# Kernel tuning notes

Measured on AMD Instinct MI355X. Metric: run time of the kernel, lower is better.

Reference implementation:

```python
import jax, jax.numpy as jnp
import numpy as np

N_EMBD = 1024
N_HEAD = 16
HEAD_DIM = N_EMBD // N_HEAD  # 64; scale = sqrt(64) = 8


def setup_inputs() -> dict:
    key = jax.random.key(0)
    k0, k1, k2, k3, k4 = jax.random.split(key, 5)
    B, T = 4, 2048
    x = jax.random.normal(k0, (B, T, N_EMBD), dtype=jnp.float32)
    # torch Linear weights are (out,in); we store (in,out) so y = x @ W + b
    W_attn = jax.random.normal(k1, (N_EMBD, 3 * N_EMBD), dtype=jnp.float32) * 0.02
    b_attn = jax.random.normal(k2, (3 * N_EMBD,), dtype=jnp.float32) * 0.02
    W_proj = jax.random.normal(k3, (N_EMBD, N_EMBD), dtype=jnp.float32) * 0.02
    b_proj = jax.random.normal(k4, (N_EMBD,), dtype=jnp.float32) * 0.02
    return {"x": x, "W_attn": W_attn, "b_attn": b_attn,
            "W_proj": W_proj, "b_proj": b_proj}


def reference(x, W_attn, b_attn, W_proj, b_proj):
    B, T, D = x.shape
    scale = 1.0 / np.float32(np.sqrt(HEAD_DIM))
    qkv = x @ W_attn + b_attn                      # [B,T,3D]
    q, k, v = jnp.split(qkv, 3, axis=-1)           # each [B,T,D]
    att = jnp.einsum('bid,bjd->bij', q, k) * scale # [B,T,T]
    causal = jnp.tril(jnp.ones((T, T), dtype=bool))
    att = jnp.where(causal[None, :, :], att, jnp.float32(-jnp.inf))
    att = jax.nn.softmax(att, axis=-1)
    y = jnp.einsum('bij,bjd->bid', att, v)         # [B,T,D]
    return y @ W_proj + b_proj
```

## Files before the change

kernel.cpp:

```cpp
#include <hip/hip_runtime.h>

typedef __attribute__((ext_vector_type(8))) short short8;
typedef __attribute__((ext_vector_type(4))) float f32x4;
typedef __attribute__((ext_vector_type(4))) unsigned short ushort4v;

struct DB0 { static constexpr int value = 0; };
struct DB1 { static constexpr int value = 1; };
struct DB2 { static constexpr int value = 2; };

__device__ __forceinline__ unsigned short f2bf(float f) {
  unsigned int u = __float_as_uint(f);
  u += 0x7fffu + ((u >> 16) & 1u);
  return (unsigned short)(u >> 16);
}
__device__ __forceinline__ float bf2f(unsigned short h) {
  return __uint_as_float(((unsigned int)h) << 16);
}

__device__ __forceinline__ void gload16(const unsigned short* g, unsigned short* l) {
  __builtin_amdgcn_global_load_lds(
      (const __attribute__((address_space(1))) unsigned int*)g,
      (__attribute__((address_space(3))) unsigned int*)l,
      16, 0, 0);
}

template <int OFF>
__device__ __forceinline__ short8 dsr(unsigned a) {
  short8 r;
  asm volatile("ds_read_b128 %0, %1 offset:%2" : "=v"(r) : "v"(a), "n"(OFF));
  return r;
}

__device__ __forceinline__ void bar() {
  asm volatile("" ::: "memory");
  __builtin_amdgcn_s_barrier();
  asm volatile("" ::: "memory");
}

__global__ __launch_bounds__(256) void prep_kernel(
    const float* __restrict__ x, unsigned short* __restrict__ xb,
    const float* __restrict__ Wa, unsigned short* __restrict__ wta,
    const float* __restrict__ Wp, unsigned short* __restrict__ wtp) {
  int b = blockIdx.x;
  int tx = threadIdx.x & 31, ty = threadIdx.x >> 5;
  if (b < 8192) {
    int i = b * 256 + threadIdx.x;
    f32x4 v = ((const f32x4*)x)[i];
    ushort4v o;
    o[0] = f2bf(v[0]); o[1] = f2bf(v[1]); o[2] = f2bf(v[2]); o[3] = f2bf(v[3]);
    ((ushort4v*)xb)[i] = o;
    return;
  }
  const float* W; unsigned short* Wt; int K, N, n0, k0;
  if (b < 8192 + 3072) {
    int bb = b - 8192; W = Wa; Wt = wta; K = 1024; N = 3072;
    n0 = (bb % 96) * 32; k0 = (bb / 96) * 32;
  } else {
    int bb = b - 11264; W = Wp; Wt = wtp; K = 1024; N = 1024;
    n0 = (bb % 32) * 32; k0 = (bb / 32) * 32;
  }
  __shared__ float tile[32][33];
#pragma unroll
  for (int j = 0; j < 32; j += 8)
    tile[ty + j][tx] = W[(size_t)(k0 + ty + j) * N + n0 + tx];
  __syncthreads();
#pragma unroll
  for (int j = 0; j < 32; j += 8)
    Wt[(size_t)(n0 + ty + j) * K + k0 + tx] = f2bf(tile[tx][ty + j]);
}

__global__ __launch_bounds__(256) void softmax_kernel(unsigned short* __restrict__ S) {
  int row = blockIdx.x * 4 + (threadIdx.x >> 6);
  int l = threadIdx.x & 63;
  int rl = row & 2047;
  int rend = ((rl >> 7) + 1) << 7;
  unsigned short* p = S + (size_t)row * 2048;
  float v[32];
  float mx = -3e38f;
#pragma unroll
  for (int i = 0; i < 4; i++) {
    int c0 = (i * 64 + l) * 8;
    if (c0 < rend) {
      short8 raw = *(const short8*)&p[c0];
#pragma unroll
      for (int j = 0; j < 8; j++) {
        v[i * 8 + j] = bf2f((unsigned short)raw[j]);
        mx = fmaxf(mx, v[i * 8 + j]);
      }
    } else {
#pragma unroll
      for (int j = 0; j < 8; j++) v[i * 8 + j] = -3e38f;
    }
  }
#pragma unroll
  for (int off = 1; off < 64; off <<= 1) mx = fmaxf(mx, __shfl_xor(mx, off));
  float s = 0.f;
#pragma unroll
  for (int i = 0; i < 32; i++) { v[i] = exp2f((v[i] - mx) * 1.44269504f); s += v[i]; }
#pragma unroll
  for (int off = 1; off < 64; off <<= 1) s += __shfl_xor(s, off);
  float inv = 1.f / s;
#pragma unroll
  for (int i = 0; i < 4; i++) {
    int c0 = (i * 64 + l) * 8;
    if (c0 < rend) {
      short8 o;
#pragma unroll
      for (int j = 0; j < 8; j++) o[j] = (short)f2bf(v[i * 8 + j] * inv);
      *(short8*)&p[c0] = o;
    }
  }
}

template <int OUTBF>
__device__ __forceinline__ void gemm_body(
    unsigned short (*lds)[16384],
    const unsigned short* __restrict__ A, int lda,
    const unsigned short* __restrict__ Bt, int ldb,
    void* __restrict__ Cv, int ldc,
    const float* __restrict__ bias, int NT, float scale, bool maskC,
    int m0, int n0) {
  const int t = threadIdx.x;
  const int lane = t & 63, wid = t >> 6;
  const int g = lane >> 4, q = lane & 15;
  const int wm = wid >> 1, wn = wid & 1;

  f32x4 acc[4][4] = {};

  {
    const int scol = ((t & 7) * 8) ^ ((t & 32) >> 1);
    const unsigned short* aS = A + (size_t)(m0 + (t >> 3)) * lda + scol;
    const unsigned short* bS = Bt + (size_t)(n0 + (t >> 3)) * ldb + scol;

    auto stage = [&](int tt) {
      unsigned short* d = &lds[tt & 1][wid * 512];
      const unsigned short* sa = aS + (size_t)tt * 64;
      const unsigned short* sb = bS + (size_t)tt * 64;
      gload16(sa, d);
      gload16(sa + (size_t)32 * lda, d + 2048);
      gload16(sa + (size_t)64 * lda, d + 4096);
      gload16(sa + (size_t)96 * lda, d + 6144);
      gload16(sb, d + 8192);
      gload16(sb + (size_t)32 * ldb, d + 10240);
      gload16(sb + (size_t)64 * ldb, d + 12288);
      gload16(sb + (size_t)96 * ldb, d + 14336);
    };

    const unsigned base =
        (unsigned)(unsigned long long)(__attribute__((address_space(3))) unsigned short*)&lds[0][0];
    const int colA = (g * 16) ^ ((q & 4) << 3);
    const unsigned aaB = base + (unsigned)((wm * 64 + q) * 128 + colA);
    const unsigned bbB = base + 16384u + (unsigned)((wn * 64 + q) * 128 + colA);

    stage(0);
    asm volatile("s_waitcnt vmcnt(0)" ::: "memory");
    bar();

    auto body = [&](auto dbc, int tt) {
      constexpr int DB = decltype(dbc)::value;
      const unsigned aa = aaB + DB * 32768u;
      const unsigned bb = bbB + DB * 32768u;
      if (tt + 1 < NT) stage(tt + 1);
      short8 aq[4][2], bq[4][2];
#pragma unroll
      for (int m = 0; m < 4; m++) {
        aq[m][0] = dsr<0>(aa + m * 2048u);
        aq[m][1] = dsr<64>(aa + m * 2048u);
      }
#pragma unroll
      for (int n = 0; n < 4; n++) {
        bq[n][0] = dsr<0>(bb + n * 2048u);
        bq[n][1] = dsr<64>(bb + n * 2048u);
      }
      asm volatile("s_waitcnt lgkmcnt(0)" ::: "memory");
      __builtin_amdgcn_sched_barrier(0);
      __builtin_amdgcn_s_setprio(1);
#pragma unroll
      for (int ks = 0; ks < 2; ks++)
#pragma unroll
        for (int m = 0; m < 4; m++)
#pragma unroll
          for (int n = 0; n < 4; n++)
            acc[m][n] = __builtin_amdgcn_mfma_f32_16x16x32_bf16(aq[m][ks], bq[n][ks], acc[m][n], 0, 0, 0);
      __builtin_amdgcn_s_setprio(0);
      __builtin_amdgcn_sched_barrier(0);
      asm volatile("s_waitcnt vmcnt(0)" ::: "memory");
      bar();
    };

    int tt = 0;
    for (; tt + 2 <= NT; tt += 2) {
      body(DB0{}, tt);
      body(DB1{}, tt + 1);
    }
    if (tt < NT) body(DB0{}, tt);
  }

#pragma unroll
  for (int n = 0; n < 4; n++) {
    int colg = n0 + wn * 64 + n * 16 + q;
    float bv = bias ? bias[colg] : 0.f;
#pragma unroll
    for (int m = 0; m < 4; m++) {
      int rowb = m0 + wm * 64 + m * 16 + g * 4;
#pragma unroll
      for (int r = 0; r < 4; r++) {
        float val = acc[m][n][r] * scale + bv;
        if (maskC && colg > rowb + r) val = -1e30f;
        if (OUTBF) {
          ((unsigned short*)Cv)[(size_t)(rowb + r) * ldc + colg] = f2bf(val);
        } else {
          ((float*)Cv)[(size_t)(rowb + r) * ldc + colg] = val;
        }
      }
    }
  }
}

__device__ __forceinline__ void gemm_body32(
    unsigned short (*lds)[8192],
    const unsigned short* __restrict__ A, int lda,
    const unsigned short* __restrict__ Bt, int ldb,
    unsigned short* __restrict__ C, int ldc,
    int NT, float scale, bool maskC, int m0, int n0) {
  const int t = threadIdx.x;
  const int lane = t & 63, wid = t >> 6;
  const int g = lane >> 4, q = lane & 15;
  const int wm = wid >> 1, wn = wid & 1;

  f32x4 acc[4][4] = {};

  {
    const int scol = ((t & 3) ^ ((t >> 3) & 3)) * 8;
    const unsigned short* aS = A + (size_t)(m0 + (t >> 2)) * lda + scol;
    const unsigned short* bS = Bt + (size_t)(n0 + (t >> 2)) * ldb + scol;

    auto stage = [&](int tt, int buf) {
      unsigned short* d = &lds[buf][wid * 512];
      const unsigned short* sa = aS + (size_t)tt * 32;
      const unsigned short* sb = bS + (size_t)tt * 32;
      gload16(sa, d);
      gload16(sa + (size_t)64 * lda, d + 2048);
      gload16(sb, d + 4096);
      gload16(sb + (size_t)64 * ldb, d + 6144);
    };

    const unsigned base =
        (unsigned)(unsigned long long)(__attribute__((address_space(3))) unsigned short*)&lds[0][0];
    const int cb = ((g ^ ((q >> 1) & 3)) << 4);
    const unsigned aaB = base + (unsigned)((wm * 64 + q) * 64 + cb);
    const unsigned bbB = base + 8192u + (unsigned)((wn * 64 + q) * 64 + cb);

    stage(0, 0);

    auto body = [&](auto dbc, int tt) {
      constexpr int DB = decltype(dbc)::value;
      if (tt + 1 < NT) {
        stage(tt + 1, (DB + 1) % 3);
        asm volatile("s_waitcnt vmcnt(4)" ::: "memory");
      } else {
        asm volatile("s_waitcnt vmcnt(0)" ::: "memory");
      }
      bar();
      const unsigned aa = aaB + DB * 16384u;
      const unsigned bb = bbB + DB * 16384u;
      short8 aq[4], bq[4];
      aq[0] = dsr<0>(aa);
      aq[1] = dsr<1024>(aa);
      aq[2] = dsr<2048>(aa);
      aq[3] = dsr<3072>(aa);
      bq[0] = dsr<0>(bb);
      bq[1] = dsr<1024>(bb);
      bq[2] = dsr<2048>(bb);
      bq[3] = dsr<3072>(bb);
      asm volatile("s_waitcnt lgkmcnt(0)" ::: "memory");
      __builtin_amdgcn_sched_barrier(0);
      __builtin_amdgcn_s_setprio(1);
#pragma unroll
      for (int m = 0; m < 4; m++)
#pragma unroll
        for (int n = 0; n < 4; n++)
          acc[m][n] = __builtin_amdgcn_mfma_f32_16x16x32_bf16(aq[m], bq[n], acc[m][n], 0, 0, 0);
      __builtin_amdgcn_s_setprio(0);
      __builtin_amdgcn_sched_barrier(0);
    };

    int tt = 0;
    for (; tt + 3 <= NT; tt += 3) {
      body(DB0{}, tt);
      body(DB1{}, tt + 1);
      body(DB2{}, tt + 2);
    }
    if (tt < NT) body(DB0{}, tt);
    if (tt + 1 < NT) body(DB1{}, tt + 1);
  }

#pragma unroll
  for (int n = 0; n < 4; n++) {
    int colg = n0 + wn * 64 + n * 16 + q;
#pragma unroll
    for (int m = 0; m < 4; m++) {
      int rowb = m0 + wm * 64 + m * 16 + g * 4;
#pragma unroll
      for (int r = 0; r < 4; r++) {
        float val = acc[m][n][r] * scale;
        if (maskC && colg > rowb + r) val = -1e30f;
        C[(size_t)(rowb + r) * ldc + colg] = f2bf(val);
      }
    }
  }
}

template <int OUTBF>
__global__ __launch_bounds__(256) void gemm128_kernel(
    const unsigned short* __restrict__ A, int lda, long long saz,
    const unsigned short* __restrict__ Bt, int ldb, long long sbz,
    void* __restrict__ Cv, int ldc, long long scz,
    const float* __restrict__ bias, int K, float scale, int causal) {
  __shared__ __align__(16) unsigned short lds[2][16384];
  int bx, by, z;
  if (causal == 4) {
    int gx = gridDim.x, gy = gridDim.y, gz = gridDim.z;
    int total = gx * gy * gz;
    int id = blockIdx.x + blockIdx.y * gx + blockIdx.z * gx * gy;
    int halfn = total >> 1;
    int half = id >= halfn;
    int r = id - half * halfn;
    bx = r % gx;
    int rest = r / gx;
    int by0 = rest % gy;
    z = rest / gy + half * (gz >> 1);
    by = half ? (gy - 1 - by0) : by0;
  } else {
    bx = blockIdx.x; by = blockIdx.y; z = blockIdx.z;
  }
  const int m0 = by * 128, n0 = bx * 128;
  int NT = K >> 6;
  if (causal == 4) NT = min(K, m0 + 128) >> 6;
  char* C = (char*)Cv + (size_t)z * scz * (OUTBF ? 2 : 4);
  gemm_body<OUTBF>(lds, A + (size_t)z * saz, lda, Bt + (size_t)z * sbz, ldb,
                   C, ldc, bias, NT, scale, false, m0, n0);
}

__global__ __launch_bounds__(256, 3) void gemm_sv_kernel(
    const unsigned short* __restrict__ qkv,
    const unsigned short* __restrict__ wtp,
    unsigned short* __restrict__ S,
    unsigned short* __restrict__ vt) {
  __shared__ __align__(16) unsigned short lds[3][8192];
  int i = blockIdx.x;
  if (i < 512) {
    int bx = i & 15, by = (i >> 4) & 7, z = i >> 7;
    gemm_body32(lds, wtp, 1024,
                qkv + 2048 + (size_t)z * 2048 * 3072, 3072,
                vt + (size_t)z * 1024 * 2048, 2048,
                32, 1.0f, false, by * 128, bx * 128);
  } else {
    int ii = i - 512;
    int z = ii / 136, tri = ii % 136;
    int by = (int)((sqrtf(8.f * tri + 1.f) - 1.f) * 0.5f);
    while ((by + 1) * (by + 2) / 2 <= tri) by++;
    while (by * (by + 1) / 2 > tri) by--;
    int bx = tri - by * (by + 1) / 2;
    gemm_body32(lds, qkv + (size_t)z * 2048 * 3072, 3072,
                qkv + 1024 + (size_t)z * 2048 * 3072, 3072,
                S + (size_t)z * 2048 * 2048, 2048,
                32, 0.125f, true, by * 128, bx * 128);
  }
}

extern "C" void kernel_launch(void* const* d_in, const int* in_sizes, int n_in,
                              void* d_out, int out_size, void* d_ws, size_t ws_size,
                              hipStream_t stream) {
  const float* x  = (const float*)d_in[0];
  const float* Wa = (const float*)d_in[1];
  const float* ba = (const float*)d_in[2];
  const float* Wp = (const float*)d_in[3];
  const float* bp = (const float*)d_in[4];
  float* out = (float*)d_out;

  char* ws = (char*)d_ws;
  unsigned short* qkv = (unsigned short*)(ws);
  unsigned short* xb  = (unsigned short*)(ws + 50331648);
  unsigned short* vt  = (unsigned short*)(ws + 50331648);
  unsigned short* wta = (unsigned short*)(ws + 67108864);
  unsigned short* S   = (unsigned short*)(ws + 73400320);
  unsigned short* wtp = (unsigned short*)(ws + 123731968);

  prep_kernel<<<12288, 256, 0, stream>>>(x, xb, Wa, wta, Wp, wtp);

  gemm128_kernel<1><<<dim3(24, 64, 1), 256, 0, stream>>>(
      xb, 1024, 0, wta, 1024, 0, qkv, 3072, 0, ba, 1024, 1.0f, 0);

  gemm_sv_kernel<<<1056, 256, 0, stream>>>(qkv, wtp, S, vt);

  softmax_kernel<<<2048, 256, 0, stream>>>(S);

  gemm128_kernel<0><<<dim3(8, 16, 4), 256, 0, stream>>>(
      S, 2048, 2048LL * 2048, vt, 2048, 2048LL * 1024,
      out, 1024, 2048LL * 1024, bp, 2048, 1.0f, 4);
}
```

Baseline: 184.5 us.

## Fuse causal softmax into the P·V projection GEMM

Removes the standalone softmax kernel and folds it into a new pv_kernel. Each block first computes the row max and sum over its causal range with an online reduction. It then exponentiates the score tiles on the fly while staging them into LDS, and applies the 1/sum normalisation plus bias in the epilogue. This saves a full read-modify-write pass over S and one launch. In exchange, every one of the 8 column blocks recomputes the row statistics and exponentials, which adds redundant reads and ALU work.

```diff
diff --git a/kernel.cpp b/kernel.cpp
--- a/kernel.cpp
+++ b/kernel.cpp
@@ -67,49 +67,6 @@
 #pragma unroll
   for (int j = 0; j < 32; j += 8)
     Wt[(size_t)(n0 + ty + j) * K + k0 + tx] = f2bf(tile[tx][ty + j]);
-}
-
-__global__ __launch_bounds__(256) void softmax_kernel(unsigned short* __restrict__ S) {
-  int row = blockIdx.x * 4 + (threadIdx.x >> 6);
-  int l = threadIdx.x & 63;
-  int rl = row & 2047;
-  int rend = ((rl >> 7) + 1) << 7;
-  unsigned short* p = S + (size_t)row * 2048;
-  float v[32];
-  float mx = -3e38f;
-#pragma unroll
-  for (int i = 0; i < 4; i++) {
-    int c0 = (i * 64 + l) * 8;
-    if (c0 < rend) {
-      short8 raw = *(const short8*)&p[c0];
-#pragma unroll
-      for (int j = 0; j < 8; j++) {
-        v[i * 8 + j] = bf2f((unsigned short)raw[j]);
-        mx = fmaxf(mx, v[i * 8 + j]);
-      }
-    } else {
-#pragma unroll
-      for (int j = 0; j < 8; j++) v[i * 8 + j] = -3e38f;
-    }
-  }
-#pragma unroll
-  for (int off = 1; off < 64; off <<= 1) mx = fmaxf(mx, __shfl_xor(mx, off));
-  float s = 0.f;
-#pragma unroll
-  for (int i = 0; i < 32; i++) { v[i] = exp2f((v[i] - mx) * 1.44269504f); s += v[i]; }
-#pragma unroll
-  for (int off = 1; off < 64; off <<= 1) s += __shfl_xor(s, off);
-  float inv = 1.f / s;
-#pragma unroll
-  for (int i = 0; i < 4; i++) {
-    int c0 = (i * 64 + l) * 8;
-    if (c0 < rend) {
-      short8 o;
-#pragma unroll
-      for (int j = 0; j < 8; j++) o[j] = (short)f2bf(v[i * 8 + j] * inv);
-      *(short8*)&p[c0] = o;
-    }
-  }
 }
 
 template <int OUTBF>
@@ -318,25 +275,9 @@
     void* __restrict__ Cv, int ldc, long long scz,
     const float* __restrict__ bias, int K, float scale, int causal) {
   __shared__ __align__(16) unsigned short lds[2][16384];
-  int bx, by, z;
-  if (causal == 4) {
-    int gx = gridDim.x, gy = gridDim.y, gz = gridDim.z;
-    int total = gx * gy * gz;
-    int id = blockIdx.x + blockIdx.y * gx + blockIdx.z * gx * gy;
-    int halfn = total >> 1;
-    int half = id >= halfn;
-    int r = id - half * halfn;
-    bx = r % gx;
-    int rest = r / gx;
-    int by0 = rest % gy;
-    z = rest / gy + half * (gz >> 1);
-    by = half ? (gy - 1 - by0) : by0;
-  } else {
-    bx = blockIdx.x; by = blockIdx.y; z = blockIdx.z;
-  }
+  int bx = blockIdx.x, by = blockIdx.y, z = blockIdx.z;
   const int m0 = by * 128, n0 = bx * 128;
   int NT = K >> 6;
-  if (causal == 4) NT = min(K, m0 + 128) >> 6;
   char* C = (char*)Cv + (size_t)z * scz * (OUTBF ? 2 : 4);
   gemm_body<OUTBF>(lds, A + (size_t)z * saz, lda, Bt + (size_t)z * sbz, ldb,
                    C, ldc, bias, NT, scale, false, m0, n0);
@@ -369,6 +310,189 @@
   }
 }
 
+__global__ __launch_bounds__(256) void pv_kernel(
+    const unsigned short* __restrict__ S,
+    const unsigned short* __restrict__ vt,
+    float* __restrict__ out,
+    const float* __restrict__ bp) {
+  __shared__ __align__(16) unsigned short lds[2][16384];
+  __shared__ float pm[2][128], ps[2][128];
+  __shared__ float mrow[128], isum[128];
+
+  int bx, by, z;
+  {
+    int gx = gridDim.x, gy = gridDim.y, gz = gridDim.z;
+    int total = gx * gy * gz;
+    int id = blockIdx.x + blockIdx.y * gx + blockIdx.z * gx * gy;
+    int halfn = total >> 1;
+    int half = id >= halfn;
+    int r = id - half * halfn;
+    bx = r % gx;
+    int rest = r / gx;
+    int by0 = rest % gy;
+    z = rest / gy + half * (gz >> 1);
+    by = half ? (gy - 1 - by0) : by0;
+  }
+  const int m0 = by * 128, n0 = bx * 128;
+  const int rend = m0 + 128;
+  const int NT = rend >> 6;
+  const unsigned short* Sz = S + (size_t)z * 2048 * 2048;
+  const unsigned short* Vz = vt + (size_t)z * 1024 * 2048;
+
+  const int t = threadIdx.x;
+  const int lane = t & 63, wid = t >> 6;
+  const int g = lane >> 4, q = lane & 15;
+  const int wm = wid >> 1, wn = wid & 1;
+  const float L2E = 1.44269504f;
+
+  {
+    int r = t & 127, half = t >> 7;
+    int rend2 = rend >> 1;
+    const unsigned short* p = Sz + (size_t)(m0 + r) * 2048 + half * rend2;
+    float m = -3e38f, s = 0.f;
+    for (int c = 0; c < rend2; c += 8) {
+      short8 raw = *(const short8*)&p[c];
+      float v[8];
+#pragma unroll
+      for (int j = 0; j < 8; j++) v[j] = bf2f((unsigned short)raw[j]);
+      float bm = v[0];
+#pragma unroll
+      for (int j = 1; j < 8; j++) bm = fmaxf(bm, v[j]);
+      if (bm > m) { s *= exp2f((m - bm) * L2E); m = bm; }
+#pragma unroll
+      for (int j = 0; j < 8; j++) s += exp2f((v[j] - m) * L2E);
+    }
+    pm[half][r] = m; ps[half][r] = s;
+  }
+  __syncthreads();
+  if (t < 128) {
+    float ma = pm[0][t], mb = pm[1][t];
+    float mm = fmaxf(ma, mb);
+    float ss = ps[0][t] * exp2f((ma - mm) * L2E) + ps[1][t] * exp2f((mb - mm) * L2E);
+    mrow[t] = mm; isum[t] = 1.f / ss;
+  }
+  __syncthreads();
+
+  f32x4 acc[4][4] = {};
+
+  {
+    const int scol = ((t & 7) * 8) ^ ((t & 32) >> 1);
+    const unsigned short* aS = Sz + (size_t)(m0 + (t >> 3)) * 2048 + scol;
+    const unsigned short* bS = Vz + (size_t)(n0 + (t >> 3)) * 2048 + scol;
+
+    float mr[4];
+#pragma unroll
+    for (int i = 0; i < 4; i++) mr[i] = mrow[(t >> 3) + i * 32];
+
+    auto stageB = [&](int tt) {
+      unsigned short* d = &lds[tt & 1][wid * 512];
+      const unsigned short* sb = bS + (size_t)tt * 64;
+      gload16(sb, d + 8192);
+      gload16(sb + (size_t)32 * 2048, d + 10240);
+      gload16(sb + (size_t)64 * 2048, d + 12288);
+      gload16(sb + (size_t)96 * 2048, d + 14336);
+    };
+    auto loadA = [&](int tt, short8* ar) {
+#pragma unroll
+      for (int i = 0; i < 4; i++)
+        ar[i] = *(const short8*)(aS + (size_t)i * 32 * 2048 + (size_t)tt * 64);
+    };
+    auto writeA = [&](int tt, short8* ar) {
+      unsigned short* d = &lds[tt & 1][wid * 512 + (lane & 63) * 8];
+#pragma unroll
+      for (int i = 0; i < 4; i++) {
+        short8 o;
+#pragma unroll
+        for (int j = 0; j < 8; j++) {
+          float v = bf2f((unsigned short)ar[i][j]);
+          o[j] = (short)f2bf(exp2f((v - mr[i]) * L2E));
+        }
+        *(short8*)&d[i * 2048] = o;
+      }
+    };
+
+    const unsigned base =
+        (unsigned)(unsigned long long)(__attribute__((address_space(3))) unsigned short*)&lds[0][0];
+    const int colA = (g * 16) ^ ((q & 4) << 3);
+    const unsigned aaB = base + (unsigned)((wm * 64 + q) * 128 + colA);
+    const unsigned bbB = base + 16384u + (unsigned)((wn * 64 + q) * 128 + colA);
+
+    {
+      short8 a0[4];
+      stageB(0);
+      loadA(0, a0);
+      asm volatile("s_waitcnt vmcnt(0)" ::: "memory");
+      writeA(0, a0);
+      asm volatile("s_waitcnt lgkmcnt(0)" ::: "memory");
+      bar();
+    }
+
+    auto body = [&](auto dbc, int tt) {
+      constexpr int DB = decltype(dbc)::value;
+      const unsigned aa = aaB + DB * 32768u;
+      const unsigned bb = bbB + DB * 32768u;
+      short8 an[4];
+      const bool more = (tt + 1 < NT);
+      if (more) {
+        stageB(tt + 1);
+        loadA(tt + 1, an);
+      }
+      short8 aq[4][2], bq[4][2];
+#pragma unroll
+      for (int m = 0; m < 4; m++) {
+        aq[m][0] = dsr<0>(aa + m * 2048u);
+        aq[m][1] = dsr<64>(aa + m * 2048u);
+      }
+#pragma unroll
+      for (int n = 0; n < 4; n++) {
+        bq[n][0] = dsr<0>(bb + n * 2048u);
+        bq[n][1] = dsr<64>(bb + n * 2048u);
+      }
+      asm volatile("s_waitcnt lgkmcnt(0)" ::: "memory");
+      __builtin_amdgcn_sched_barrier(0);
+      __builtin_amdgcn_s_setprio(1);
+#pragma unroll
+      for (int ks = 0; ks < 2; ks++)
+#pragma unroll
+        for (int m = 0; m < 4; m++)
+#pragma unroll
+          for (int n = 0; n < 4; n++)
+            acc[m][n] = __builtin_amdgcn_mfma_f32_16x16x32_bf16(aq[m][ks], bq[n][ks], acc[m][n], 0, 0, 0);
+      __builtin_amdgcn_s_setprio(0);
+      __builtin_amdgcn_sched_barrier(0);
+      asm volatile("s_waitcnt vmcnt(0)" ::: "memory");
+      if (more) {
+        writeA(tt + 1, an);
+        asm volatile("s_waitcnt lgkmcnt(0)" ::: "memory");
+      }
+      bar();
+    };
+
+    int tt = 0;
+    for (; tt + 2 <= NT; tt += 2) {
+      body(DB0{}, tt);
+      body(DB1{}, tt + 1);
+    }
+    if (tt < NT) body(DB0{}, tt);
+  }
+
+  float* oz = out + (size_t)z * 2048 * 1024;
+#pragma unroll
+  for (int n = 0; n < 4; n++) {
+    int colg = n0 + wn * 64 + n * 16 + q;
+    float bv = bp[colg];
+#pragma unroll
+    for (int m = 0; m < 4; m++) {
+      int rowl = wm * 64 + m * 16 + g * 4;
+#pragma unroll
+      for (int r = 0; r < 4; r++) {
+        float val = acc[m][n][r] * isum[rowl + r] + bv;
+        oz[(size_t)(m0 + rowl + r) * 1024 + colg] = val;
+      }
+    }
+  }
+}
+
 extern "C" void kernel_launch(void* const* d_in, const int* in_sizes, int n_in,
                               void* d_out, int out_size, void* d_ws, size_t ws_size,
                               hipStream_t stream) {
@@ -394,9 +518,5 @@
 
   gemm_sv_kernel<<<1056, 256, 0, stream>>>(qkv, wtp, S, vt);
 
-  softmax_kernel<<<2048, 256, 0, stream>>>(S);
-
-  gemm128_kernel<0><<<dim3(8, 16, 4), 256, 0, stream>>>(
-      S, 2048, 2048LL * 2048, vt, 2048, 2048LL * 1024,
-      out, 1024, 2048LL * 1024, bp, 2048, 1.0f, 4);
-}
+  pv_kernel<<<dim3(8, 16, 4), 256, 0, stream>>>(S, vt, out, bp);
+}
```

New measurement: 248.4 us. +34.6%, slower.
